# Kernel optimization log

Hardware: AMD Instinct MI355X
Metric: run time of the kernel (lower is better)

Reference implementation:

```python
import jax, jax.numpy as jnp
import numpy as np

T = 3072          # packed tokens (B==1 varlen)
DIM = 1024        # model_dim
H = 8             # num_heads
D = 128           # head_dim
GATE_IN = 16      # gate projections read first 16 channels of x
ATTN_SCALE = 0.1  # Yarn attn_scale
BM = 1408         # sliding-window size (block_size * ws)


def _rms_norm(x, eps=1e-6):
    return x * jax.lax.rsqrt(jnp.mean(x * x, axis=-1, keepdims=True) + eps)


def _rotary(x, cos, sin):
    # x: [B,T,H,D]; cos/sin: [T,D//2]
    c = cos[None, :x.shape[1], None, :]
    s = sin[None, :x.shape[1], None, :]
    x1, x2 = jnp.split(x, 2, axis=-1)
    return jnp.concatenate([x1 * c + x2 * s, -x1 * s + x2 * c], axis=-1)


def setup_inputs() -> dict:
    key = jax.random.key(0)
    ks = jax.random.split(key, 6)
    x = jax.random.normal(ks[0], (1, T, DIM), dtype=jnp.float32)
    qkvo_w = 0.02 * jax.random.normal(ks[1], (4 * DIM, DIM), dtype=jnp.float32)
    sa_lambdas = jnp.ones((2,), dtype=jnp.float32)
    ve = 0.5 * jax.random.normal(ks[2], (T, DIM), dtype=jnp.float32)
    attn_gate_w = 0.1 * jax.random.normal(ks[3], (H, GATE_IN), dtype=jnp.float32)
    ve_gate_w = 0.1 * jax.random.normal(ks[4], (H, GATE_IN), dtype=jnp.float32)
    # Yarn rotary tables: half the freq channels are zero (NoPE half)
    angular_freq = (1.0 / 1024.0) ** jnp.linspace(0, 1, D // 4, dtype=jnp.float32)
    angular_freq = jnp.concatenate([angular_freq, jnp.zeros(D // 4, dtype=jnp.float32)])
    theta = jnp.arange(T, dtype=jnp.float32)[:, None] * angular_freq[None, :]
    cos, sin = jnp.cos(theta), jnp.sin(theta)
    # two packed sequences of length T//2 (cu_seqlens = [0, T//2, T])
    seg_ids = jnp.concatenate([jnp.zeros(T // 2, jnp.int32), jnp.ones(T // 2, jnp.int32)])
    return {"x": x, "qkvo_w": qkvo_w, "sa_lambdas": sa_lambdas, "ve": ve,
            "attn_gate_w": attn_gate_w, "ve_gate_w": ve_gate_w,
            "cos": cos, "sin": sin, "seg_ids": seg_ids, "bm_size": BM}


def reference(x, qkvo_w, sa_lambdas, ve, attn_gate_w, ve_gate_w, cos, sin, seg_ids, bm_size):
    B, Tt, dim = x.shape
    nh = attn_gate_w.shape[0]
    hd = dim // nh
    # fused qkv projection with learned lambda scaling
    qkv = x @ (sa_lambdas[0] * qkvo_w[:3 * dim]).T              # [B,T,3*dim]
    qkv = qkv.reshape(B, Tt, 3 * nh, hd)
    q, k, v = jnp.split(qkv, 3, axis=2)                          # each [B,T,H,D]
    q, k = _rms_norm(q), _rms_norm(k)
    q, k = _rotary(q, cos, sin), _rotary(k, cos, sin)
    # key_offset: channels [D/4:D/2] and [3D/4:D] take previous token's keys
    k_prev = jnp.concatenate([k[:, :1], k[:, :-1]], axis=1)
    k = jnp.concatenate([k[..., :hd // 4], k_prev[..., hd // 4:hd // 2],
                         k[..., hd // 2:3 * hd // 4], k_prev[..., 3 * hd // 4:]], axis=-1)
    # value-embedding gate: 2*sigmoid(x[:,:,:16] @ W^T)
    ve_gate = 2.0 * jax.nn.sigmoid(x[..., :ve_gate_w.shape[-1]] @ ve_gate_w.T)  # [B,T,H]
    v = v + ve_gate[..., None] * ve.reshape(B, Tt, nh, hd)
    # windowed causal varlen attention (dense reference for flash_attn_varlen)
    scores = jnp.einsum('bthd,bshd->bhts', q, k) * ATTN_SCALE
    t_idx = jnp.arange(Tt)
    mask = ((t_idx[None, :] <= t_idx[:, None])
            & (t_idx[None, :] >= t_idx[:, None] - bm_size)
            & (seg_ids[None, :] == seg_ids[:, None]))
    scores = jnp.where(mask[None, None], scores, -jnp.inf)
    p = jax.nn.softmax(scores, axis=-1)
    y = jnp.einsum('bhts,bshd->bthd', p, v)
    # attention output gate
    gate = jax.nn.sigmoid(x[..., :attn_gate_w.shape[-1]] @ attn_gate_w.T)      # [B,T,H]
    y = y * gate[..., None]
    y = y.reshape(B, Tt, dim)
    return y @ (sa_lambdas[1] * qkvo_w[3 * dim:]).T
```

## Files before the change

kernel.cpp:

```cpp
#include <hip/hip_runtime.h>
#include <hip/hip_bf16.h>
#include <stdint.h>

#define TSEQ 3072
#define DIMM 1024
#define NH   8
#define HD   128
#define QBLK 32
#define BM   1408
#define CHUNK 384
#define NQB  (TSEQ / QBLK)
#define NCMAX 5

typedef float f32x4 __attribute__((ext_vector_type(4)));
typedef short s16x8 __attribute__((ext_vector_type(8)));
typedef unsigned short u16;

static __device__ __forceinline__ u16 f2b(float f) {
  union { float f; unsigned u; } a; a.f = f;
  unsigned r = a.u + 0x7FFFu + ((a.u >> 16) & 1u);
  return (u16)(r >> 16);
}
static __device__ __forceinline__ float b2f(u16 u) {
  union { unsigned u; float f; } a; a.u = ((unsigned)u) << 16;
  return a.f;
}
static __device__ __forceinline__ void gload_lds16(const void* g, void* l) {
  __builtin_amdgcn_global_load_lds(
      (const __attribute__((address_space(1))) unsigned int*)(unsigned long long)g,
      (__attribute__((address_space(3))) unsigned int*)(unsigned long long)l,
      16, 0, 0);
}
static __device__ __forceinline__ void bar() {
  asm volatile("" ::: "memory");
  __builtin_amdgcn_s_barrier();
  asm volatile("" ::: "memory");
}
#define SWAIT(n) asm volatile("s_waitcnt vmcnt(" #n ")" ::: "memory")

__global__ __launch_bounds__(256) void k_convert(
    const float* __restrict__ x, const float* __restrict__ w,
    const float* __restrict__ lam,
    u16* __restrict__ xb, u16* __restrict__ wb)
{
  const int NX = TSEQ * DIMM;
  const int NW = 4 * DIMM * DIMM;
  const float l0 = lam[0], l1 = lam[1];
  const int n4 = (NX + NW) >> 2;
  for (int j = blockIdx.x * 256 + threadIdx.x; j < n4; j += gridDim.x * 256) {
    const int e = j << 2;
    float4 v; u16* dst; float s;
    if (e < NX) { v = *(const float4*)(x + e); dst = xb + e; s = 1.f; }
    else {
      const int we = e - NX;
      v = *(const float4*)(w + we);
      dst = wb + we;
      s = (we < 3 * DIMM * DIMM) ? l0 : l1;
    }
    dst[0] = f2b(v.x * s); dst[1] = f2b(v.y * s);
    dst[2] = f2b(v.z * s); dst[3] = f2b(v.w * s);
  }
}

__global__ __launch_bounds__(256) void k_gemm_nt(
    const u16* __restrict__ A, const u16* __restrict__ B,
    float* __restrict__ C, int M, int N, int K)
{
  __shared__ u16 As[2][128 * 64];
  __shared__ u16 Bs[2][128 * 64];
  const int tid = threadIdx.x;
  const int lane = tid & 63, wv = tid >> 6;
  const int m0 = blockIdx.y * 128, n0 = blockIdx.x * 128;
  const int wm = (wv >> 1) * 64, wn = (wv & 1) * 64;
  const int c0 = lane & 15, r0 = (lane >> 4) * 4, koff = (lane >> 4) * 8;

  f32x4 acc[4][4];
  #pragma unroll
  for (int i = 0; i < 4; i++)
    #pragma unroll
    for (int j = 0; j < 4; j++) acc[i][j] = (f32x4){0.f, 0.f, 0.f, 0.f};

  const int srow  = tid >> 3;
  const int scolb = (tid & 7) * 16;

  auto stage = [&](int buf, int kt) {
    #pragma unroll
    for (int i = 0; i < 4; i++) {
      const int row = srow + i * 32;
      const int scb = scolb ^ ((row & 7) << 4);
      const int ldst = row * 128 + scolb;
      gload_lds16(A + (size_t)(m0 + row) * K + kt + (scb >> 1), (char*)As[buf] + ldst);
      gload_lds16(B + (size_t)(n0 + row) * K + kt + (scb >> 1), (char*)Bs[buf] + ldst);
    }
  };

  stage(0, 0);
  int cur = 0;
  for (int kt = 0; kt < K; kt += 64) {
    if (kt + 64 < K) {
      stage(cur ^ 1, kt + 64);
      SWAIT(8);
    } else {
      SWAIT(0);
    }
    bar();

    #pragma unroll
    for (int kk = 0; kk < 2; kk++) {
      s16x8 af[4], bf[4];
      #pragma unroll
      for (int i = 0; i < 4; i++) {
        const int ar = wm + i * 16 + c0;
        const int br = wn + i * 16 + c0;
        const int cb = (kk * 32 + koff) * 2;
        af[i] = *(const s16x8*)((const char*)As[cur] + ar * 128 + (cb ^ ((ar & 7) << 4)));
        bf[i] = *(const s16x8*)((const char*)Bs[cur] + br * 128 + (cb ^ ((br & 7) << 4)));
      }
      #pragma unroll
      for (int i = 0; i < 4; i++)
        #pragma unroll
        for (int j = 0; j < 4; j++)
          acc[i][j] = __builtin_amdgcn_mfma_f32_16x16x32_bf16(af[i], bf[j], acc[i][j], 0, 0, 0);
    }

    bar();
    cur ^= 1;
  }

  #pragma unroll
  for (int i = 0; i < 4; i++)
    #pragma unroll
    for (int j = 0; j < 4; j++) {
      float* cp = C + (size_t)(m0 + wm + i * 16 + r0) * N + n0 + wn + j * 16 + c0;
      #pragma unroll
      for (int r = 0; r < 4; r++) cp[(size_t)r * N] = acc[i][j][r];
    }
}

__global__ __launch_bounds__(256) void k_prep(
    const float* __restrict__ qkv, const float* __restrict__ x,
    const float* __restrict__ ve, const float* __restrict__ cosb,
    const float* __restrict__ sinb, const float* __restrict__ gwa,
    const float* __restrict__ gwv, const int* __restrict__ seg,
    u16* __restrict__ Qg, u16* __restrict__ Kg, u16* __restrict__ VTg,
    float* __restrict__ gateA, int* __restrict__ segb)
{
  __shared__ u16 vtile[64][130];
  const int tid = threadIdx.x;
  const int lane = tid & 63, w = tid >> 6;
  const int h = blockIdx.y;
  const int t0 = blockIdx.x * 64;

  if (h == 0 && t0 == 0 && tid == 0) {
    const int sv = seg[0];
    int lo = 1, hi = TSEQ;
    while (lo < hi) { const int mid = (lo + hi) >> 1; if (seg[mid] == sv) lo = mid + 1; else hi = mid; }
    segb[0] = lo;
  }

  for (int it = 0; it < 16; ++it) {
    const int tt = it * 4 + w;
    const int t = t0 + tt;
    const int tp = (t == 0) ? 0 : t - 1;

    const float* qrow = qkv + (size_t)t * (3 * DIMM) + h * HD;
    const float* krow = qrow + DIMM;
    const float* vrow = qrow + 2 * DIMM;
    const float* prow = qkv + (size_t)tp * (3 * DIMM) + DIMM + h * HD;

    float q1 = qrow[lane], q2 = qrow[lane + 64];
    float k1 = krow[lane], k2 = krow[lane + 64];
    float p1 = prow[lane], p2 = prow[lane + 64];

    float sq = q1 * q1 + q2 * q2, sk = k1 * k1 + k2 * k2, sp = p1 * p1 + p2 * p2;
    #pragma unroll
    for (int m = 1; m < 64; m <<= 1) {
      sq += __shfl_xor(sq, m, 64);
      sk += __shfl_xor(sk, m, 64);
      sp += __shfl_xor(sp, m, 64);
    }
    const float rq = rsqrtf(sq * (1.f / 128.f) + 1e-6f);
    const float rk = rsqrtf(sk * (1.f / 128.f) + 1e-6f);
    const float rp = rsqrtf(sp * (1.f / 128.f) + 1e-6f);
    q1 *= rq; q2 *= rq; k1 *= rk; k2 *= rk; p1 *= rp; p2 *= rp;

    const float c  = cosb[t * 64 + lane],  s  = sinb[t * 64 + lane];
    const float cp = cosb[tp * 64 + lane], spv = sinb[tp * 64 + lane];
    const float qo1 =  q1 * c + q2 * s,   qo2 = -q1 * s + q2 * c;
    const float ko1 =  k1 * c + k2 * s,   ko2 = -k1 * s + k2 * c;
    const float po1 =  p1 * cp + p2 * spv, po2 = -p1 * spv + p2 * cp;
    const float m1 = (lane < 32) ? ko1 : po1;
    const float m2 = (lane < 32) ? ko2 : po2;

    const size_t qkbase = ((size_t)h * TSEQ + t) * HD + lane;
    Qg[qkbase] = f2b(qo1 * 0.1f); Qg[qkbase + 64] = f2b(qo2 * 0.1f);
    Kg[qkbase] = f2b(m1);  Kg[qkbase + 64] = f2b(m2);

    float dv = 0.f, da = 0.f;
    #pragma unroll
    for (int g = 0; g < 16; g++) {
      const float xv = x[(size_t)t * DIMM + g];
      dv += xv * gwv[h * 16 + g];
      da += xv * gwa[h * 16 + g];
    }
    const float vg = 2.f / (1.f + __expf(-dv));
    const float v1 = vrow[lane]      + vg * ve[(size_t)t * DIMM + h * HD + lane];
    const float v2 = vrow[lane + 64] + vg * ve[(size_t)t * DIMM + h * HD + lane + 64];
    vtile[tt][lane] = f2b(v1); vtile[tt][lane + 64] = f2b(v2);
    if (lane == 0) gateA[h * TSEQ + t] = 1.f / (1.f + __expf(-da));
  }
  __syncthreads();
  #pragma unroll
  for (int rep = 0; rep < 4; ++rep) {
    const int d = rep * 32 + (tid >> 3);
    const int cc = (tid & 7) * 8;
    s16x8 v;
    #pragma unroll
    for (int j = 0; j < 8; j++) ((u16*)&v)[j] = vtile[cc + j][d];
    *(s16x8*)(VTg + ((size_t)h * HD + d) * TSEQ + t0 + cc) = v;
  }
}

__global__ __launch_bounds__(128) void k_attn(
    const u16* __restrict__ Qg, const u16* __restrict__ Kg,
    const u16* __restrict__ VTg, const int* __restrict__ segb,
    u16* __restrict__ Opart, float* __restrict__ Mp, float* __restrict__ Lp)
{
  __shared__ u16 Ks[2][64 * HD];
  __shared__ u16 Vs[HD * 64];
  __shared__ u16 Ps[2][16 * 64];

  const int h  = blockIdx.x;
  const int qb = blockIdx.y;
  const int rc = blockIdx.z;
  const int q0 = qb * QBLK;

  const int c_lo = ((q0 - BM) > 0 ? (q0 - BM) : 0) / CHUNK;
  const int c_hi = (q0 + QBLK - 1) / CHUNK;
  if (rc > c_hi - c_lo) return;
  const int c = c_lo + rc;

  const int tid = threadIdx.x, lane = tid & 63, wv = tid >> 6;
  const int qw = q0 + wv * 16;
  const int r0 = (lane >> 4) * 4, c0 = lane & 15;
  const int koff = (lane >> 4) * 8;

  const int b = segb[0];

  int loop_lo = q0 - BM; if (loop_lo < 0) loop_lo = 0;
  if (q0 >= b) loop_lo = (loop_lo > b) ? loop_lo : b;
  int s_lo = loop_lo & ~63;
  const int cs = c * CHUNK;
  if (s_lo < cs) s_lo = cs;
  int s_hi = q0 + QBLK;
  if (s_hi > cs + CHUNK) s_hi = cs + CHUNK;

  s16x8 qf[4];
  {
    const u16* qp = Qg + ((size_t)h * TSEQ + qw + c0) * HD + koff;
    #pragma unroll
    for (int kk = 0; kk < 4; kk++) qf[kk] = *(const s16x8*)(qp + kk * 32);
  }

  int qt[4]; int qub[4];
  #pragma unroll
  for (int r = 0; r < 4; r++) { qt[r] = qw + r0 + r; qub[r] = (qt[r] >= b) ? 1 : 0; }

  f32x4 o[8];
  #pragma unroll
  for (int i = 0; i < 8; i++) o[i] = (f32x4){0.f, 0.f, 0.f, 0.f};
  float mrow[4] = {-1e30f, -1e30f, -1e30f, -1e30f};
  float lrow[4] = {0.f, 0.f, 0.f, 0.f};

  auto stageK = [&](int buf, int s0k) {
    #pragma unroll
    for (int i = 0; i < 8; i++) {
      const int L = tid * 16 + i * 2048;
      const int kr = L >> 8;
      const int kc = (L & 255) ^ ((kr & 7) << 4);
      gload_lds16(Kg + ((size_t)h * TSEQ + s0k + kr) * HD + (kc >> 1), (char*)Ks[buf] + L);
    }
  };
  auto stageV = [&](int s0v) {
    #pragma unroll
    for (int i = 0; i < 8; i++) {
      const int L = tid * 16 + i * 2048;
      const int vr = L >> 7;
      const int vc = (L & 127) ^ ((vr & 7) << 4);
      gload_lds16(VTg + ((size_t)h * HD + vr) * TSEQ + s0v + (vc >> 1), (char*)Vs + L);
    }
  };

  if (s_lo < s_hi) {
    stageK(0, s_lo);
    int cur = 0;
    for (int s0 = s_lo; s0 < s_hi; s0 += 64) {
      bar();
      stageV(s0);
      int sn = s0 + 64; if (sn >= s_hi) sn = s0;
      stageK(cur ^ 1, sn);
      SWAIT(16);
      bar();

      const char* kbase = (const char*)Ks[cur];
      f32x4 sv[4];
      #pragma unroll
      for (int n = 0; n < 4; n++) {
        sv[n] = (f32x4){0.f, 0.f, 0.f, 0.f};
        const int krow = n * 16 + c0;
        #pragma unroll
        for (int kk = 0; kk < 4; kk++) {
          const int kbyte = (krow << 8) + ((((kk * 32 + koff) << 1)) ^ ((krow & 7) << 4));
          const s16x8 kf = *(const s16x8*)(kbase + kbyte);
          sv[n] = __builtin_amdgcn_mfma_f32_16x16x32_bf16(qf[kk], kf, sv[n], 0, 0, 0);
        }
      }

      const bool keys_same_seg_as_q =
          ((s0 >= b) && (qw >= b)) || ((s0 + 63 < b) && (qw + 15 < b));
      const bool interior = (s0 + 64 <= qw) && (s0 >= qw + 15 - BM) && keys_same_seg_as_q;
      if (!interior) {
        #pragma unroll
        for (int n = 0; n < 4; n++) {
          const int key = s0 + n * 16 + c0;
          const int kub = (key >= b) ? 1 : 0;
          #pragma unroll
          for (int r = 0; r < 4; r++) {
            const bool ok = (key <= qt[r]) && (key >= qt[r] - BM) && (kub == qub[r]);
            sv[n][r] = ok ? sv[n][r] : -1e30f;
          }
        }
      }

      float pm[4];
      #pragma unroll
      for (int r = 0; r < 4; r++)
        pm[r] = fmaxf(fmaxf(sv[0][r], sv[1][r]), fmaxf(sv[2][r], sv[3][r]));
      #pragma unroll
      for (int m = 1; m < 16; m <<= 1)
        #pragma unroll
        for (int r = 0; r < 4; r++) pm[r] = fmaxf(pm[r], __shfl_xor(pm[r], m, 64));

      int need = 0;
      #pragma unroll
      for (int r = 0; r < 4; r++) need |= (pm[r] > mrow[r] + 8.f) ? 1 : 0;
      if (__any(need)) {
        #pragma unroll
        for (int r = 0; r < 4; r++) {
          const float mn = fmaxf(mrow[r], pm[r]);
          const float scl = __expf(mrow[r] - mn);
          mrow[r] = mn;
          lrow[r] *= scl;
          #pragma unroll
          for (int i = 0; i < 8; i++) o[i][r] *= scl;
        }
      }

      u16 pb[4][4];
      #pragma unroll
      for (int n = 0; n < 4; n++)
        #pragma unroll
        for (int r = 0; r < 4; r++) {
          const float p = (sv[n][r] < -0.5e30f) ? 0.f : __expf(sv[n][r] - mrow[r]);
          lrow[r] += p;
          pb[n][r] = f2b(p);
        }

      char* pbase = (char*)Ps[wv];
      #pragma unroll
      for (int n = 0; n < 4; n++)
        #pragma unroll
        for (int r = 0; r < 4; r++) {
          const int row = r0 + r;
          const int byt = (row << 7) + ((((n * 16 + c0) << 1)) ^ ((row & 7) << 4));
          *(u16*)(pbase + byt) = pb[n][r];
        }

      SWAIT(8);
      bar();

      #pragma unroll
      for (int kc = 0; kc < 2; kc++) {
        const int pbyte = (c0 << 7) + ((((kc * 32 + koff) << 1)) ^ ((c0 & 7) << 4));
        const s16x8 pf = *(const s16x8*)(pbase + pbyte);
        #pragma unroll
        for (int nf = 0; nf < 8; nf++) {
          const int vrow = nf * 16 + c0;
          const int vbyte = (vrow << 7) + ((((kc * 32 + koff) << 1)) ^ ((vrow & 7) << 4));
          const s16x8 vf = *(const s16x8*)((const char*)Vs + vbyte);
          o[nf] = __builtin_amdgcn_mfma_f32_16x16x32_bf16(pf, vf, o[nf], 0, 0, 0);
        }
      }
      cur ^= 1;
    }
    SWAIT(0);
  }

  #pragma unroll
  for (int m = 1; m < 16; m <<= 1)
    #pragma unroll
    for (int r = 0; r < 4; r++) lrow[r] += __shfl_xor(lrow[r], m, 64);

  const int pidx = (h * NQB + qb) * NCMAX + rc;
  #pragma unroll
  for (int r = 0; r < 4; r++) {
    const int wrow = wv * 16 + r0 + r;
    u16* op = Opart + (size_t)pidx * (32 * 128) + wrow * 128;
    #pragma unroll
    for (int nf = 0; nf < 8; nf++) op[nf * 16 + c0] = f2b(o[nf][r]);
    if (c0 == 0) {
      Mp[pidx * 32 + wrow] = mrow[r];
      Lp[pidx * 32 + wrow] = lrow[r];
    }
  }
}

__global__ __launch_bounds__(256) void k_merge(
    const u16* __restrict__ Opart, const float* __restrict__ Mp,
    const float* __restrict__ Lp, const float* __restrict__ gateA,
    u16* __restrict__ Y)
{
  const int qb = blockIdx.x, h = blockIdx.y;
  const int q0 = qb * QBLK;
  const int c_lo = ((q0 - BM) > 0 ? (q0 - BM) : 0) / CHUNK;
  const int c_hi = (q0 + QBLK - 1) / CHUNK;
  const int nc = c_hi - c_lo + 1;

  const int tid = threadIdx.x;
  const int row = tid >> 3;
  const int dg = (tid & 7) * 16;
  const int qt = q0 + row;
  const int base = (h * NQB + qb) * NCMAX;

  float m = -1e30f;
  for (int rc = 0; rc < nc; rc++) {
    const float mc = Mp[(base + rc) * 32 + row];
    m = fmaxf(m, mc);
  }
  float l = 0.f;
  float acc[16];
  #pragma unroll
  for (int j = 0; j < 16; j++) acc[j] = 0.f;
  for (int rc = 0; rc < nc; rc++) {
    const float mc = Mp[(base + rc) * 32 + row];
    const float w = __expf(mc - m);
    l += w * Lp[(base + rc) * 32 + row];
    const u16* op = Opart + (size_t)(base + rc) * (32 * 128) + row * 128 + dg;
    const s16x8 v0 = *(const s16x8*)(op);
    const s16x8 v1 = *(const s16x8*)(op + 8);
    #pragma unroll
    for (int j = 0; j < 8; j++) {
      acc[j]     += w * b2f(((const u16*)&v0)[j]);
      acc[j + 8] += w * b2f(((const u16*)&v1)[j]);
    }
  }
  const float inv = (l > 0.f) ? (gateA[h * TSEQ + qt] / l) : 0.f;
  u16* yp = Y + (size_t)qt * DIMM + h * HD + dg;
  #pragma unroll
  for (int j = 0; j < 16; j++) yp[j] = f2b(acc[j] * inv);
}

extern "C" void kernel_launch(void* const* d_in, const int* in_sizes, int n_in,
                              void* d_out, int out_size, void* d_ws, size_t ws_size,
                              hipStream_t stream) {
  const float* x    = (const float*)d_in[0];
  const float* qkvo = (const float*)d_in[1];
  const float* lam  = (const float*)d_in[2];
  const float* ve   = (const float*)d_in[3];
  const float* gwa  = (const float*)d_in[4];
  const float* gwv  = (const float*)d_in[5];
  const float* cosb = (const float*)d_in[6];
  const float* sinb = (const float*)d_in[7];
  const int*   seg  = (const int*)d_in[8];
  float* out = (float*)d_out;

  char* ws = (char*)d_ws;
  size_t off = 0;
  auto alloc = [&](size_t bytes) -> void* {
    void* p = ws + off;
    off += (bytes + 255) & ~(size_t)255;
    return p;
  };
  u16*   xb    = (u16*)alloc((size_t)TSEQ * DIMM * 2);
  u16*   wb    = (u16*)alloc((size_t)4 * DIMM * DIMM * 2);
  float* qkv   = (float*)alloc((size_t)TSEQ * 3 * DIMM * 4);
  u16*   Qg    = (u16*)alloc((size_t)NH * TSEQ * HD * 2);
  u16*   Kg    = (u16*)alloc((size_t)NH * TSEQ * HD * 2);
  u16*   VTg   = (u16*)alloc((size_t)NH * HD * TSEQ * 2);
  float* gateA = (float*)alloc((size_t)NH * TSEQ * 4);
  u16*   Yg    = (u16*)alloc((size_t)TSEQ * DIMM * 2);
  int*   segb  = (int*)alloc(256);

  u16*   Opart = (u16*)qkv;
  float* Mp    = (float*)((char*)qkv + (size_t)NH * NQB * NCMAX * 32 * 128 * 2);
  float* Lp    = Mp + (size_t)NH * NQB * NCMAX * 32;

  k_convert<<<2048, 256, 0, stream>>>(x, qkvo, lam, xb, wb);
  k_gemm_nt<<<dim3(24, 24), 256, 0, stream>>>(xb, wb, qkv, TSEQ, 3 * DIMM, DIMM);
  k_prep<<<dim3(TSEQ / 64, NH), 256, 0, stream>>>(qkv, x, ve, cosb, sinb, gwa, gwv, seg,
                                                  Qg, Kg, VTg, gateA, segb);
  k_attn<<<dim3(NH, NQB, NCMAX), 128, 0, stream>>>(Qg, Kg, VTg, segb, Opart, Mp, Lp);
  k_merge<<<dim3(NQB, NH), 256, 0, stream>>>(Opart, Mp, Lp, gateA, Yg);
  k_gemm_nt<<<dim3(DIMM / 128, 24), 256, 0, stream>>>(Yg, wb + (size_t)3 * DIMM * DIMM, out, TSEQ, DIMM, DIMM);
}
```

Before: 209.9 us.

## Load V fragments directly to registers in attention and halve prep tile

The attention kernel no longer stages V into shared memory. Each wave now reads its V MFMA fragments straight from global memory into registers, and the K prefetch for the next tile is issued after those loads, which removes one barrier per key tile and the V LDS buffer. In exchange each lane holds 16 extra vector registers and issues more scattered global reads, with each wave re-reading V instead of sharing it. The prep kernel is also retiled to 32 tokens per block with an unrolled loop to launch more blocks.

After: 231.2 us. 1.1x slower.

```diff
diff --git a/kernel.cpp b/kernel.cpp
--- a/kernel.cpp
+++ b/kernel.cpp
@@ -37,6 +37,7 @@
   asm volatile("" ::: "memory");
 }
 #define SWAIT(n) asm volatile("s_waitcnt vmcnt(" #n ")" ::: "memory")
+#define CFENCE() asm volatile("" ::: "memory")
 
 __global__ __launch_bounds__(256) void k_convert(
     const float* __restrict__ x, const float* __restrict__ w,
@@ -145,11 +146,11 @@
     u16* __restrict__ Qg, u16* __restrict__ Kg, u16* __restrict__ VTg,
     float* __restrict__ gateA, int* __restrict__ segb)
 {
-  __shared__ u16 vtile[64][130];
+  __shared__ u16 vtile[32][130];
   const int tid = threadIdx.x;
   const int lane = tid & 63, w = tid >> 6;
   const int h = blockIdx.y;
-  const int t0 = blockIdx.x * 64;
+  const int t0 = blockIdx.x * 32;
 
   if (h == 0 && t0 == 0 && tid == 0) {
     const int sv = seg[0];
@@ -158,7 +159,8 @@
     segb[0] = lo;
   }
 
-  for (int it = 0; it < 16; ++it) {
+  #pragma unroll
+  for (int it = 0; it < 8; ++it) {
     const int tt = it * 4 + w;
     const int t = t0 + tt;
     const int tp = (t == 0) ? 0 : t - 1;
@@ -211,9 +213,9 @@
   }
   __syncthreads();
   #pragma unroll
-  for (int rep = 0; rep < 4; ++rep) {
-    const int d = rep * 32 + (tid >> 3);
-    const int cc = (tid & 7) * 8;
+  for (int rep = 0; rep < 2; ++rep) {
+    const int d = rep * 64 + (tid >> 2);
+    const int cc = (tid & 3) * 8;
     s16x8 v;
     #pragma unroll
     for (int j = 0; j < 8; j++) ((u16*)&v)[j] = vtile[cc + j][d];
@@ -227,7 +229,6 @@
     u16* __restrict__ Opart, float* __restrict__ Mp, float* __restrict__ Lp)
 {
   __shared__ u16 Ks[2][64 * HD];
-  __shared__ u16 Vs[HD * 64];
   __shared__ u16 Ps[2][16 * 64];
 
   const int h  = blockIdx.x;
@@ -272,6 +273,8 @@
   float mrow[4] = {-1e30f, -1e30f, -1e30f, -1e30f};
   float lrow[4] = {0.f, 0.f, 0.f, 0.f};
 
+  const u16* __restrict__ Vb = VTg + (size_t)h * HD * TSEQ;
+
   auto stageK = [&](int buf, int s0k) {
     #pragma unroll
     for (int i = 0; i < 8; i++) {
@@ -281,25 +284,12 @@
       gload_lds16(Kg + ((size_t)h * TSEQ + s0k + kr) * HD + (kc >> 1), (char*)Ks[buf] + L);
     }
   };
-  auto stageV = [&](int s0v) {
-    #pragma unroll
-    for (int i = 0; i < 8; i++) {
-      const int L = tid * 16 + i * 2048;
-      const int vr = L >> 7;
-      const int vc = (L & 127) ^ ((vr & 7) << 4);
-      gload_lds16(VTg + ((size_t)h * HD + vr) * TSEQ + s0v + (vc >> 1), (char*)Vs + L);
-    }
-  };
 
   if (s_lo < s_hi) {
     stageK(0, s_lo);
     int cur = 0;
     for (int s0 = s_lo; s0 < s_hi; s0 += 64) {
-      bar();
-      stageV(s0);
-      int sn = s0 + 64; if (sn >= s_hi) sn = s0;
-      stageK(cur ^ 1, sn);
-      SWAIT(16);
+      SWAIT(0);
       bar();
 
       const char* kbase = (const char*)Ks[cur];
@@ -315,6 +305,19 @@
           sv[n] = __builtin_amdgcn_mfma_f32_16x16x32_bf16(qf[kk], kf, sv[n], 0, 0, 0);
         }
       }
+
+      CFENCE();
+      s16x8 vf[2][8];
+      #pragma unroll
+      for (int kc = 0; kc < 2; kc++)
+        #pragma unroll
+        for (int nf = 0; nf < 8; nf++)
+          vf[kc][nf] = *(const s16x8*)(Vb + (size_t)(nf * 16 + c0) * TSEQ + s0 + kc * 32 + koff);
+      CFENCE();
+
+      const int sn = s0 + 64;
+      if (sn < s_hi) stageK(cur ^ 1, sn);
+      CFENCE();
 
       const bool keys_same_seg_as_q =
           ((s0 >= b) && (qw >= b)) || ((s0 + 63 < b) && (qw + 15 < b));
@@ -366,6 +369,8 @@
           pb[n][r] = f2b(p);
         }
 
+      SWAIT(8);
+
       char* pbase = (char*)Ps[wv];
       #pragma unroll
       for (int n = 0; n < 4; n++)
@@ -375,21 +380,13 @@
           const int byt = (row << 7) + ((((n * 16 + c0) << 1)) ^ ((row & 7) << 4));
           *(u16*)(pbase + byt) = pb[n][r];
         }
-
-      SWAIT(8);
-      bar();
-
       #pragma unroll
       for (int kc = 0; kc < 2; kc++) {
         const int pbyte = (c0 << 7) + ((((kc * 32 + koff) << 1)) ^ ((c0 & 7) << 4));
         const s16x8 pf = *(const s16x8*)(pbase + pbyte);
         #pragma unroll
-        for (int nf = 0; nf < 8; nf++) {
-          const int vrow = nf * 16 + c0;
-          const int vbyte = (vrow << 7) + ((((kc * 32 + koff) << 1)) ^ ((vrow & 7) << 4));
-          const s16x8 vf = *(const s16x8*)((const char*)Vs + vbyte);
-          o[nf] = __builtin_amdgcn_mfma_f32_16x16x32_bf16(pf, vf, o[nf], 0, 0, 0);
-        }
+        for (int nf = 0; nf < 8; nf++)
+          o[nf] = __builtin_amdgcn_mfma_f32_16x16x32_bf16(pf, vf[kc][nf], o[nf], 0, 0, 0);
       }
       cur ^= 1;
     }
@@ -497,7 +494,7 @@
 
   k_convert<<<2048, 256, 0, stream>>>(x, qkvo, lam, xb, wb);
   k_gemm_nt<<<dim3(24, 24), 256, 0, stream>>>(xb, wb, qkv, TSEQ, 3 * DIMM, DIMM);
-  k_prep<<<dim3(TSEQ / 64, NH), 256, 0, stream>>>(qkv, x, ve, cosb, sinb, gwa, gwv, seg,
+  k_prep<<<dim3(TSEQ / 32, NH), 256, 0, stream>>>(qkv, x, ve, cosb, sinb, gwa, gwv, seg,
                                                   Qg, Kg, VTg, gateA, segb);
   k_attn<<<dim3(NH, NQB, NCMAX), 128, 0, stream>>>(Qg, Kg, VTg, segb, Opart, Mp, Lp);
   k_merge<<<dim3(NQB, NH), 256, 0, stream>>>(Opart, Mp, Lp, gateA, Yg);
```
